# Kernel optimization log

Measured on AMD Instinct MI355X. Metric: run time of the kernel, lower is better.

The kernel has to match this reference:

```python
import jax, jax.numpy as jnp
import numpy as np

N, E, B = 50000, 800000, 128
NF, ED, HID, HEADS, DH, OUT, L = 7, 2, 128, 4, 32, 64, 3
EPS = 1e-5
NEG_SLOPE = 0.2


def _layer_norm(x, g, b):
    mu = jnp.mean(x, axis=-1, keepdims=True)
    v = jnp.mean((x - mu) ** 2, axis=-1, keepdims=True)
    return g * (x - mu) / jnp.sqrt(v + EPS) + b


def setup_inputs() -> dict:
    key = jax.random.key(0)
    ks = jax.random.split(key, 32)
    s = 0.05
    inp = {
        "x": jax.random.normal(ks[0], (N, NF), jnp.float32),
        "edge_index": jax.random.randint(ks[1], (2, E), 0, N, jnp.int32),
        "edge_attr": jax.random.uniform(ks[2], (E, ED), jnp.float32),
        "batch": jnp.sort(jax.random.randint(ks[3], (N,), 0, B, jnp.int32)),
        # node encoder
        "enc_W": jax.random.normal(ks[4], (NF, HID)) * (1.0 / np.sqrt(NF)),
        "enc_b": jnp.zeros((HID,)),
        "enc_g": jnp.ones((HID,)),
        "enc_bb": jnp.zeros((HID,)),
        # GATv2 layers (stacked over L)
        "gat_Wsrc": jax.random.normal(ks[5], (L, HID, HID)) * (1.0 / np.sqrt(HID)),
        "gat_Wdst": jax.random.normal(ks[6], (L, HID, HID)) * (1.0 / np.sqrt(HID)),
        "gat_We": jax.random.normal(ks[7], (L, ED, HID)) * (1.0 / np.sqrt(ED)),
        "gat_att": jax.random.normal(ks[8], (L, HEADS, DH)) * s,
        "gat_bias": jnp.zeros((L, HID)),
        # GraphNorm per layer
        "gn_w": jnp.ones((L, HID)),
        "gn_b": jnp.zeros((L, HID)),
        "gn_s": jnp.ones((L, HID)),  # mean_scale
        # attention pooling
        "pool_W1": jax.random.normal(ks[9], (HID, HID)) * (1.0 / np.sqrt(HID)),
        "pool_b1": jnp.zeros((HID,)),
        "pool_W2": jax.random.normal(ks[10], (HID, 1)) * (1.0 / np.sqrt(HID)),
        # output mapper
        "map_W1": jax.random.normal(ks[11], (HID, HID)) * (1.0 / np.sqrt(HID)),
        "map_b1": jnp.zeros((HID,)),
        "map_g": jnp.ones((HID,)),
        "map_bb": jnp.zeros((HID,)),
        "map_W2": jax.random.normal(ks[12], (HID, OUT)) * (1.0 / np.sqrt(HID)),
        "map_b2": jnp.zeros((OUT,)),
    }
    return inp


def _segment_softmax(scores, seg, num_seg):
    # scores: [E2, HEADS], seg: [E2] destination node ids
    m = jax.ops.segment_max(scores, seg, num_segments=num_seg)
    ex = jnp.exp(scores - m[seg])
    denom = jax.ops.segment_sum(ex, seg, num_segments=num_seg)
    return ex / denom[seg]


def _gatv2(x, src, dst, ea, Wsrc, Wdst, We, att, bias):
    e2 = src.shape[0]
    xl = (x @ Wsrc)[src].reshape(e2, HEADS, DH)   # lin_l(x_j), source
    xr = (x @ Wdst)[dst].reshape(e2, HEADS, DH)   # lin_r(x_i), target
    ee = (ea @ We).reshape(e2, HEADS, DH)
    z = jax.nn.leaky_relu(xl + xr + ee, NEG_SLOPE)
    score = jnp.einsum("ehd,hd->eh", z, att)
    alpha = _segment_softmax(score, dst, N)       # softmax over incoming edges
    msg = (xl * alpha[:, :, None]).reshape(e2, HID)
    out = jax.ops.segment_sum(msg, dst, num_segments=N)
    return out + bias


def _graph_norm(x, batch, w, b, scale):
    cnt = jax.ops.segment_sum(jnp.ones((N,), x.dtype), batch, num_segments=B)
    cnt = jnp.maximum(cnt, 1.0)[:, None]
    mean = jax.ops.segment_sum(x, batch, num_segments=B) / cnt
    xc = x - scale * mean[batch]
    var = jax.ops.segment_sum(xc * xc, batch, num_segments=B) / cnt
    return w * xc / jnp.sqrt(var[batch] + EPS) + b


def reference(x, edge_index, edge_attr, batch, enc_W, enc_b, enc_g, enc_bb,
              gat_Wsrc, gat_Wdst, gat_We, gat_att, gat_bias, gn_w, gn_b, gn_s,
              pool_W1, pool_b1, pool_W2, map_W1, map_b1, map_g, map_bb,
              map_W2, map_b2):
    # node encoder: Linear -> ReLU -> LayerNorm
    h = _layer_norm(jax.nn.relu(x @ enc_W + enc_b), enc_g, enc_bb)

    # add self loops; self-loop edge_attr = mean of edge_attr (PyG fill_value='mean')
    loop = jnp.arange(N, dtype=edge_index.dtype)
    src = jnp.concatenate([edge_index[0], loop])
    dst = jnp.concatenate([edge_index[1], loop])
    ea_mean = jnp.mean(edge_attr, axis=0)
    ea = jnp.concatenate([edge_attr, jnp.broadcast_to(ea_mean, (N, ED))], axis=0)

    for i in range(L):
        out = _gatv2(h, src, dst, ea, gat_Wsrc[i], gat_Wdst[i], gat_We[i],
                     gat_att[i], gat_bias[i])
        out = out + h  # residual (in_dim == out_dim -> Identity proj)
        out = _graph_norm(out, batch, gn_w[i], gn_b[i], gn_s[i])
        h = jax.nn.elu(out)

    node_emb = h
    # attention pooling: softmax over ALL nodes (dim=0, as in source)
    scores = jnp.tanh(h @ pool_W1 + pool_b1) @ pool_W2          # [N, 1]
    weights = jax.nn.softmax(scores, axis=0)
    g = jax.ops.segment_sum(h * weights, batch, num_segments=B)  # [B, HID]

    # output mapper (dropout inactive at eval)
    g = _layer_norm(jax.nn.relu(g @ map_W1 + map_b1), map_g, map_bb)
    graph_emb = g @ map_W2 + map_b2
    return graph_emb, node_emb
```

## Files before the change

kernel.cpp:

```cpp
#include <hip/hip_runtime.h>
#include <hip/hip_bf16.h>

typedef __hip_bfloat16 bf16;
typedef __attribute__((ext_vector_type(8))) short short8;
typedef __attribute__((ext_vector_type(4))) float float4v;

#define Nn   50000
#define Ee   800000
#define E2   850000
#define Bb   128
#define NFd  7
#define HID  128
#define OUTD 64
#define EPS  1e-5f
#define SLOPE 0.2f
#define LOG2E 1.4426950408889634f
#define NSTRIP 3125
#define NPAIR  1563

#define MFMA16(a,b,c) __builtin_amdgcn_mfma_f32_16x16x32_bf16(a,b,c,0,0,0)

__device__ __forceinline__ float lane_bcast(float v, int l){
  return __int_as_float(__builtin_amdgcn_readlane(__float_as_int(v), l));
}
__device__ __forceinline__ float wred_sum(float v){
  #pragma unroll
  for (int o=32;o;o>>=1) v += __shfl_xor(v, o, 64);
  return v;
}
__device__ __forceinline__ float dpp_ror_add(float x, const int ctrl_is_below);
#define DPP_ROR_ADD(x, ctrl) \
  ((x) + __int_as_float(__builtin_amdgcn_update_dpp(0, __float_as_int(x), (ctrl), 0xf, 0xf, false)))
__device__ __forceinline__ float red16_dpp(float x){
  x = DPP_ROR_ADD(x, 0x121);
  x = DPP_ROR_ADD(x, 0x122);
  x = DPP_ROR_ADD(x, 0x124);
  x = DPP_ROR_ADD(x, 0x128);
  return x;
}
__device__ __forceinline__ unsigned fkey(float f){
  unsigned u = __float_as_uint(f);
  return (u & 0x80000000u) ? ~u : (u | 0x80000000u);
}
__device__ __forceinline__ float fkeyinv(unsigned k){
  unsigned u = (k & 0x80000000u) ? (k ^ 0x80000000u) : ~k;
  return __uint_as_float(u);
}
__device__ __forceinline__ float tanh_fast(float x){
  float e = __expf(fminf(fmaxf(2.f*x, -30.f), 30.f));
  return (e-1.f)/(e+1.f);
}
__device__ __forceinline__ float bf_lo(unsigned u){ return __uint_as_float(u<<16); }
__device__ __forceinline__ float bf_hi(unsigned u){ return __uint_as_float(u & 0xffff0000u); }
__device__ __forceinline__ unsigned short f2bs(float f){
  bf16 h = __float2bfloat16(f);
  return *reinterpret_cast<unsigned short*>(&h);
}
__device__ __forceinline__ unsigned pack2(float a, float b){
  return (unsigned)f2bs(a) | ((unsigned)f2bs(b) << 16);
}
__device__ __forceinline__ int xcd_swizzle(int bid, int nwg){
  int q = nwg >> 3, r = nwg & 7;
  int x = bid & 7, i = bid >> 3;
  return (x < r ? x*(q+1) : r*(q+1) + (x-r)*q) + i;
}

__global__ __launch_bounds__(256) void k_encoder(
    const float* __restrict__ x, const float* __restrict__ W, const float* __restrict__ b,
    const float* __restrict__ g, const float* __restrict__ bbv,
    float* __restrict__ h, unsigned* __restrict__ hbu){
  int wv = (blockIdx.x*blockDim.x + threadIdx.x) >> 6;
  if (wv >= Nn) return;
  int lane = threadIdx.x & 63;
  int d0 = 2*lane, d1 = d0+1;
  float y0 = b[d0], y1 = b[d1];
  #pragma unroll
  for (int i=0;i<NFd;++i){
    float xv = x[wv*NFd + i];
    y0 = fmaf(xv, W[i*HID + d0], y0);
    y1 = fmaf(xv, W[i*HID + d1], y1);
  }
  y0 = fmaxf(y0, 0.f); y1 = fmaxf(y1, 0.f);
  float mu = wred_sum(y0+y1) * (1.f/HID);
  float c0 = y0-mu, c1 = y1-mu;
  float var = wred_sum(c0*c0 + c1*c1) * (1.f/HID);
  float rs = rsqrtf(var + EPS);
  float v0 = g[d0]*c0*rs + bbv[d0];
  float v1 = g[d1]*c1*rs + bbv[d1];
  *(float2*)(h + (size_t)wv*HID + d0) = make_float2(v0, v1);
  hbu[(size_t)wv*64 + lane] = pack2(v0, v1);
}

__global__ void k_ea_mean(const float* __restrict__ ea, float* __restrict__ eam){
  int tid = blockIdx.x*blockDim.x + threadIdx.x;
  const float2* ea2 = (const float2*)ea;
  float a0=0.f, a1=0.f;
  for (int e=tid; e<Ee; e += gridDim.x*blockDim.x){
    float2 v = ea2[e];
    a0 += v.x; a1 += v.y;
  }
  a0 = wred_sum(a0); a1 = wred_sum(a1);
  if ((threadIdx.x & 63)==0){
    atomicAdd(&eam[0], a0*(1.f/Ee));
    atomicAdd(&eam[1], a1*(1.f/Ee));
  }
}

__global__ void k_deg(const int* __restrict__ ei, int* __restrict__ deg){
  int e = blockIdx.x*blockDim.x + threadIdx.x;
  if (e >= E2) return;
  int d = (e < Ee) ? ei[Ee + e] : (e - Ee);
  atomicAdd(&deg[d], 1);
}

__global__ __launch_bounds__(1024) void k_scan(const int* __restrict__ deg,
    int* __restrict__ offs, int* __restrict__ cursor){
  __shared__ int wsum[16];
  __shared__ int tot_s;
  __shared__ int carry_s;
  int t = threadIdx.x, lane = t & 63, wid = t >> 6;
  if (t==0) carry_s = 0;
  __syncthreads();
  for (int base=0; base<Nn; base += 4096){
    int i0 = base + t*4;
    int v0=0,v1=0,v2=0,v3=0;
    if (i0+3 < Nn){
      int4 qv = *(const int4*)(deg + i0);
      v0=qv.x; v1=qv.y; v2=qv.z; v3=qv.w;
    } else {
      if (i0   < Nn) v0 = deg[i0];
      if (i0+1 < Nn) v1 = deg[i0+1];
      if (i0+2 < Nn) v2 = deg[i0+2];
      if (i0+3 < Nn) v3 = deg[i0+3];
    }
    int tot = v0+v1+v2+v3;
    int x = tot;
    #pragma unroll
    for (int o=1;o<64;o<<=1){ int u = __shfl_up(x, o, 64); if (lane >= o) x += u; }
    if (lane==63) wsum[wid] = x;
    __syncthreads();
    if (t==0){ int s=0; for (int k=0;k<16;++k){ int tv=wsum[k]; wsum[k]=s; s+=tv; } tot_s = s; }
    __syncthreads();
    int excl = carry_s + wsum[wid] + (x - tot);
    int p0 = excl, p1 = excl+v0, p2 = p1+v1, p3 = p2+v2;
    if (i0+3 < Nn){
      *(int4*)(offs + i0)   = make_int4(p0,p1,p2,p3);
      *(int4*)(cursor + i0) = make_int4(p0,p1,p2,p3);
    } else {
      if (i0   < Nn){ offs[i0]  =p0; cursor[i0]  =p0; }
      if (i0+1 < Nn){ offs[i0+1]=p1; cursor[i0+1]=p1; }
      if (i0+2 < Nn){ offs[i0+2]=p2; cursor[i0+2]=p2; }
      if (i0+3 < Nn){ offs[i0+3]=p3; cursor[i0+3]=p3; }
    }
    __syncthreads();
    if (t==0) carry_s += tot_s;
    __syncthreads();
  }
  if (t==0) offs[Nn] = carry_s;
}

__global__ void k_scatter(const int* __restrict__ ei, const float* __restrict__ ea,
    const float* __restrict__ eam, int* __restrict__ cursor,
    int* __restrict__ csrc, float2* __restrict__ cea){
  int e = blockIdx.x*blockDim.x + threadIdx.x;
  if (e >= E2) return;
  int s, d; float a0, a1;
  if (e < Ee){
    s = ei[e]; d = ei[Ee + e];
    float2 v = ((const float2*)ea)[e];
    a0 = v.x; a1 = v.y;
  } else {
    s = d = e - Ee; a0 = eam[0]; a1 = eam[1];
  }
  int pos = atomicAdd(&cursor[d], 1);
  csrc[pos] = s;
  cea[pos] = make_float2(a0, a1);
}

__global__ void k_gstart(const int* __restrict__ batch, int* __restrict__ gstart){
  int n = blockIdx.x*blockDim.x + threadIdx.x;
  if (n >= Nn) return;
  int bc = batch[n];
  int bp = (n==0) ? -1 : batch[n-1];
  for (int b = bp+1; b <= bc; ++b) gstart[b] = n;
  if (n == Nn-1){ for (int b = bc+1; b <= Bb; ++b) gstart[b] = Nn; }
}

__global__ __launch_bounds__(256) void k_dualgemm(
    const unsigned* __restrict__ hbu,
    const float* __restrict__ Wsrc, const float* __restrict__ Wdst,
    unsigned* __restrict__ hsb, float* __restrict__ hd){
  __shared__ unsigned short wt[256*HID];
  #pragma unroll
  for (int iter=0; iter<64; ++iter){
    int idx = iter*256 + threadIdx.x;
    int n = idx & 255, kp = idx >> 8;
    const float* Wp = (n < 128) ? Wsrc : (Wdst - 128);
    float w0 = Wp[(2*kp)*HID + n];
    float w1 = Wp[(2*kp+1)*HID + n];
    int byt = (n*256 + kp*4) ^ ((n&7)<<4);
    *(unsigned*)((char*)wt + byt) = pack2(w0, w1);
  }
  __syncthreads();
  int wid = threadIdx.x >> 6, lane = threadIdx.x & 63;
  int q = lane >> 4, c = lane & 15;
  const unsigned short* hb = (const unsigned short*)hbu;
  for (int pr = blockIdx.x*4 + wid; pr < NPAIR; pr += gridDim.x*4){
    int p0 = 2*pr, p1 = 2*pr + 1;
    bool v1 = (p1 < NSTRIP);
    int node0 = p0*16 + c;
    int node1 = v1 ? (p1*16 + c) : node0;
    short8 bf0[4], bf1[4];
    const unsigned short* hp0 = hb + (size_t)node0*HID + q*8;
    const unsigned short* hp1 = hb + (size_t)node1*HID + q*8;
    #pragma unroll
    for (int s=0;s<4;++s){
      bf0[s] = *(const short8*)(hp0 + s*32);
      bf1[s] = *(const short8*)(hp1 + s*32);
    }
    #pragma unroll 4
    for (int t=0;t<16;++t){
      float4v ac0 = {0.f,0.f,0.f,0.f}, ac1 = {0.f,0.f,0.f,0.f};
      #pragma unroll
      for (int s=0;s<4;++s){
        int row = t*16 + c;
        int byt = (row*256 + s*64 + q*16) ^ ((row&7)<<4);
        short8 af = *(const short8*)((const char*)wt + byt);
        ac0 = MFMA16(af, bf0[s], ac0);
        ac1 = MFMA16(af, bf1[s], ac1);
      }
      if (t < 8){
        int co = t*8 + q*2;
        *(uint2*)(hsb + (size_t)node0*64 + co) =
            make_uint2(pack2(ac0[0],ac0[1]), pack2(ac0[2],ac0[3]));
        if (v1) *(uint2*)(hsb + (size_t)node1*64 + co) =
            make_uint2(pack2(ac1[0],ac1[1]), pack2(ac1[2],ac1[3]));
      } else {
        int dd = (t-8)*16 + q*4;
        *(float4*)(hd + (size_t)node0*HID + dd) = make_float4(ac0[0],ac0[1],ac0[2],ac0[3]);
        if (v1) *(float4*)(hd + (size_t)node1*HID + dd) = make_float4(ac1[0],ac1[1],ac1[2],ac1[3]);
      }
    }
  }
}

__global__ __launch_bounds__(256) void k_edge(const unsigned* __restrict__ hsb,
    float* __restrict__ hdio, const float* __restrict__ h,
    const int* __restrict__ csrc, const float2* __restrict__ cea,
    const int* __restrict__ offs, const float* __restrict__ We,
    const float* __restrict__ att, const float* __restrict__ bias){
  int bid = xcd_swizzle(blockIdx.x, gridDim.x);
  int n = (bid*256 + (int)threadIdx.x) >> 6;
  if (n >= Nn) return;
  int lane = threadIdx.x & 63;
  int d0 = 2*lane, d1 = d0+1;
  float we00 = We[d0],       we01 = We[d1];
  float we10 = We[HID+d0],   we11 = We[HID+d1];
  float at0  = att[(lane>>4)*32 + (d0&31)] * LOG2E;
  float at1  = att[(lane>>4)*32 + (d1&31)] * LOG2E;
  float2 xr = *(const float2*)(hdio + (size_t)n*HID + d0);
  int e0 = offs[n], e1 = offs[n+1];

  unsigned xu = hsb[((unsigned)csrc[e0]<<6) + lane];
  float2 ev = cea[e0];
  float xl0 = bf_lo(xu), xl1 = bf_hi(xu);
  float z0 = fmaf(ev.y, we10, fmaf(ev.x, we00, xl0 + xr.x));
  float z1 = fmaf(ev.y, we11, fmaf(ev.x, we01, xl1 + xr.y));
  z0 = fmaxf(z0, SLOPE*z0); z1 = fmaxf(z1, SLOPE*z1);
  float m = red16_dpp(fmaf(z1, at1, z0*at0));
  float ssum = 1.f, acc0 = xl0, acc1 = xl1;

  int e = e0 + 1;
  int rem = e1 - e;
  int npair = rem >> 1;
  int sA, sB; float2 eA, eB; unsigned xA, xB;
  if (npair > 0){
    sA = csrc[e]; sB = csrc[e+1];
    eA = cea[e];  eB = cea[e+1];
    xA = hsb[((unsigned)sA<<6) + lane];
    xB = hsb[((unsigned)sB<<6) + lane];
  }
  for (int i = 0; i < npair; ++i){
    int sA_n=0, sB_n=0; float2 eA_n, eB_n; unsigned xA_n=0, xB_n=0;
    if (i+1 < npair){
      int en = e + 2;
      sA_n = csrc[en]; sB_n = csrc[en+1];
      eA_n = cea[en];  eB_n = cea[en+1];
      xA_n = hsb[((unsigned)sA_n<<6) + lane];
      xB_n = hsb[((unsigned)sB_n<<6) + lane];
    }
    float xA0 = bf_lo(xA), xA1 = bf_hi(xA);
    float xB0 = bf_lo(xB), xB1 = bf_hi(xB);
    float zA0 = fmaf(eA.y, we10, fmaf(eA.x, we00, xA0 + xr.x));
    float zA1 = fmaf(eA.y, we11, fmaf(eA.x, we01, xA1 + xr.y));
    float zB0 = fmaf(eB.y, we10, fmaf(eB.x, we00, xB0 + xr.x));
    float zB1 = fmaf(eB.y, we11, fmaf(eB.x, we01, xB1 + xr.y));
    zA0 = fmaxf(zA0, SLOPE*zA0); zA1 = fmaxf(zA1, SLOPE*zA1);
    zB0 = fmaxf(zB0, SLOPE*zB0); zB1 = fmaxf(zB1, SLOPE*zB1);
    float scA = red16_dpp(fmaf(zA1, at1, zA0*at0));
    float scB = red16_dpp(fmaf(zB1, at1, zB0*at0));
    float pA = exp2f(scA - m);
    float pB = exp2f(scB - m);
    ssum += pA + pB;
    acc0 = fmaf(pA, xA0, fmaf(pB, xB0, acc0));
    acc1 = fmaf(pA, xA1, fmaf(pB, xB1, acc1));
    e += 2;
    sA=sA_n; sB=sB_n; eA=eA_n; eB=eB_n; xA=xA_n; xB=xB_n;
  }
  if (rem & 1){
    int s = csrc[e1-1]; float2 eav = cea[e1-1];
    unsigned xt = hsb[((unsigned)s<<6) + lane];
    float x0 = bf_lo(xt), x1 = bf_hi(xt);
    float t0 = fmaf(eav.y, we10, fmaf(eav.x, we00, x0 + xr.x));
    float t1 = fmaf(eav.y, we11, fmaf(eav.x, we01, x1 + xr.y));
    t0 = fmaxf(t0, SLOPE*t0); t1 = fmaxf(t1, SLOPE*t1);
    float sc = red16_dpp(fmaf(t1, at1, t0*at0));
    float p = exp2f(sc - m);
    ssum += p;
    acc0 = fmaf(p, x0, acc0);
    acc1 = fmaf(p, x1, acc1);
  }
  float inv = 1.f/ssum;
  float o0 = acc0*inv + bias[d0] + h[(size_t)n*HID + d0];
  float o1 = acc1*inv + bias[d1] + h[(size_t)n*HID + d1];
  *(float2*)(hdio + (size_t)n*HID + d0) = make_float2(o0, o1);
}

__global__ __launch_bounds__(128) void k_gn_reduce(const float* __restrict__ out,
    const int* __restrict__ gstart, float* __restrict__ gsum_, float* __restrict__ gsq_){
  int b = blockIdx.x >> 4, sub = blockIdx.x & 15;
  int ns = gstart[b], ne = gstart[b+1];
  int d = threadIdx.x;
  float s = 0.f, qq = 0.f;
  for (int n = ns + sub; n < ne; n += 16){
    float v = out[(size_t)n*HID + d];
    s += v; qq = fmaf(v, v, qq);
  }
  atomicAdd(&gsum_[b*HID + d], s);
  atomicAdd(&gsq_[b*HID + d], qq);
}

__global__ __launch_bounds__(256) void k_gn_apply(const float* __restrict__ out,
    const float* __restrict__ gsum_, const float* __restrict__ gsq_,
    const int* __restrict__ gstart, const int* __restrict__ batch,
    const float* __restrict__ gw, const float* __restrict__ gb,
    const float* __restrict__ gs, float* __restrict__ h,
    unsigned* __restrict__ hbu, float* __restrict__ emb){
  int n = (blockIdx.x*blockDim.x + threadIdx.x) >> 6;
  if (n >= Nn) return;
  int lane = threadIdx.x & 63;
  int b = batch[n];
  float icnt = 1.f / fmaxf((float)(gstart[b+1]-gstart[b]), 1.f);
  int d0 = 2*lane, d1 = d0+1;
  float2 x = *(const float2*)(out + (size_t)n*HID + d0);
  float mean0 = gsum_[b*HID+d0]*icnt, mean1 = gsum_[b*HID+d1]*icnt;
  float ms0 = mean0*gs[d0], ms1 = mean1*gs[d1];
  float var0 = gsq_[b*HID+d0]*icnt - ms0*(2.f*mean0 - ms0);
  float var1 = gsq_[b*HID+d1]*icnt - ms1*(2.f*mean1 - ms1);
  float rs0 = rsqrtf(fmaxf(var0, 0.f) + EPS);
  float rs1 = rsqrtf(fmaxf(var1, 0.f) + EPS);
  float y0 = gw[d0]*(x.x - ms0)*rs0 + gb[d0];
  float y1 = gw[d1]*(x.y - ms1)*rs1 + gb[d1];
  y0 = (y0 > 0.f) ? y0 : (__expf(y0) - 1.f);
  y1 = (y1 > 0.f) ? y1 : (__expf(y1) - 1.f);
  *(float2*)(h + (size_t)n*HID + d0) = make_float2(y0, y1);
  hbu[(size_t)n*64 + lane] = pack2(y0, y1);
  if (emb) *(float2*)(emb + (size_t)n*HID + d0) = make_float2(y0, y1);
}

__global__ __launch_bounds__(256) void k_pool_score(
    const unsigned* __restrict__ hbu,
    const float* __restrict__ W1, const float* __restrict__ b1, const float* __restrict__ W2,
    float* __restrict__ score, unsigned* __restrict__ mkey){
  __shared__ unsigned short wt[HID*HID];
  __shared__ float b1l[HID], w2l[HID];
  #pragma unroll
  for (int iter=0; iter<32; ++iter){
    int idx = iter*256 + threadIdx.x;
    int n = idx & 127, kp = idx >> 7;
    float w0 = W1[(2*kp)*HID + n];
    float w1 = W1[(2*kp+1)*HID + n];
    int byt = (n*256 + kp*4) ^ ((n&7)<<4);
    *(unsigned*)((char*)wt + byt) = pack2(w0, w1);
  }
  if (threadIdx.x < HID){ b1l[threadIdx.x] = b1[threadIdx.x]; w2l[threadIdx.x] = W2[threadIdx.x]; }
  __syncthreads();
  int wid = threadIdx.x >> 6, lane = threadIdx.x & 63;
  int q = lane >> 4, c = lane & 15;
  const unsigned short* hb = (const unsigned short*)hbu;
  float bmax = -1e30f;
  for (int p = blockIdx.x*4 + wid; p < NSTRIP; p += gridDim.x*4){
    int node = p*16 + c;
    short8 bf[4];
    const unsigned short* hp = hb + (size_t)node*HID + q*8;
    #pragma unroll
    for (int s=0;s<4;++s) bf[s] = *(const short8*)(hp + s*32);
    float part = 0.f;
    #pragma unroll
    for (int t=0;t<8;++t){
      float4v ac = {0.f,0.f,0.f,0.f};
      #pragma unroll
      for (int s=0;s<4;++s){
        int row = t*16 + c;
        int byt = (row*256 + s*64 + q*16) ^ ((row&7)<<4);
        ac = MFMA16(*(const short8*)((const char*)wt + byt), bf[s], ac);
      }
      int dim = t*16 + q*4;
      #pragma unroll
      for (int r=0;r<4;++r)
        part += tanh_fast(ac[r] + b1l[dim+r]) * w2l[dim+r];
    }
    part += __shfl_xor(part, 16, 64);
    part += __shfl_xor(part, 32, 64);
    if (q==0) score[node] = part;
    bmax = fmaxf(bmax, part);
  }
  #pragma unroll
  for (int o=32;o;o>>=1) bmax = fmaxf(bmax, __shfl_xor(bmax, o, 64));
  if (lane==0) atomicMax(mkey, fkey(bmax));
}

__global__ __launch_bounds__(128) void k_pool_reduce(const float* __restrict__ h,
    const float* __restrict__ score, const unsigned* __restrict__ mkey,
    const int* __restrict__ gstart, float* __restrict__ gsum, float* __restrict__ total){
  int b = blockIdx.x >> 4, sub = blockIdx.x & 15;
  int ns = gstart[b], ne = gstart[b+1];
  float mx = fkeyinv(*mkey);
  int d = threadIdx.x;
  float acc = 0.f, es = 0.f;
  for (int n = ns + sub; n < ne; n += 16){
    float ev = __expf(score[n] - mx);
    acc = fmaf(ev, h[(size_t)n*HID + d], acc);
    if (d==0) es += ev;
  }
  atomicAdd(&gsum[b*HID + d], acc);
  if (d==0) atomicAdd(total, es);
}

__global__ __launch_bounds__(64) void k_mapper(const float* __restrict__ gsum,
    const float* __restrict__ total,
    const float* __restrict__ W1, const float* __restrict__ b1,
    const float* __restrict__ g,  const float* __restrict__ bbv,
    const float* __restrict__ W2, const float* __restrict__ b2v,
    float* __restrict__ out0){
  int b = blockIdx.x, lane = threadIdx.x;
  float inv = 1.f/(*total);
  int d0 = 2*lane, d1 = d0+1;
  float gv0 = gsum[b*HID + d0]*inv, gv1 = gsum[b*HID + d1]*inv;
  float a0 = b1[d0], a1 = b1[d1];
  for (int i=0;i<HID;++i){
    float hv = lane_bcast((i&1) ? gv1 : gv0, i>>1);
    a0 = fmaf(hv, W1[i*HID + d0], a0);
    a1 = fmaf(hv, W1[i*HID + d1], a1);
  }
  a0 = fmaxf(a0, 0.f); a1 = fmaxf(a1, 0.f);
  float mu = wred_sum(a0+a1) * (1.f/HID);
  float c0 = a0-mu, c1 = a1-mu;
  float var = wred_sum(c0*c0 + c1*c1) * (1.f/HID);
  float rs = rsqrtf(var + EPS);
  float l0 = g[d0]*c0*rs + bbv[d0];
  float l1 = g[d1]*c1*rs + bbv[d1];
  float acc = b2v[lane];
  for (int j=0;j<HID;++j){
    float lv = lane_bcast((j&1) ? l1 : l0, j>>1);
    acc = fmaf(lv, W2[j*OUTD + lane], acc);
  }
  out0[b*OUTD + lane] = acc;
}

extern "C" void kernel_launch(void* const* d_in, const int* in_sizes, int n_in,
                              void* d_out, int out_size, void* d_ws, size_t ws_size,
                              hipStream_t stream){
  const float* x     = (const float*)d_in[0];
  const int*   ei    = (const int*)  d_in[1];
  const float* ea    = (const float*)d_in[2];
  const int*   batch = (const int*)  d_in[3];
  const float* encW  = (const float*)d_in[4];
  const float* encb  = (const float*)d_in[5];
  const float* encg  = (const float*)d_in[6];
  const float* encbb = (const float*)d_in[7];
  const float* gWsrc = (const float*)d_in[8];
  const float* gWdst = (const float*)d_in[9];
  const float* gWe   = (const float*)d_in[10];
  const float* gatt  = (const float*)d_in[11];
  const float* gbias = (const float*)d_in[12];
  const float* gnw   = (const float*)d_in[13];
  const float* gnb   = (const float*)d_in[14];
  const float* gns   = (const float*)d_in[15];
  const float* pW1   = (const float*)d_in[16];
  const float* pb1   = (const float*)d_in[17];
  const float* pW2   = (const float*)d_in[18];
  const float* mW1   = (const float*)d_in[19];
  const float* mb1   = (const float*)d_in[20];
  const float* mg    = (const float*)d_in[21];
  const float* mbb   = (const float*)d_in[22];
  const float* mW2   = (const float*)d_in[23];
  const float* mb2   = (const float*)d_in[24];

  char* w = (char*)d_ws;
  size_t off = 0;
  auto alloc = [&](size_t bytes)->char*{
    char* p = w + off;
    off += (bytes + 255) & ~(size_t)255;
    return p;
  };
  float*    h      = (float*)   alloc((size_t)Nn*HID*4);
  unsigned* hbu    = (unsigned*)alloc((size_t)Nn*64*4);
  unsigned* hsb    = (unsigned*)alloc((size_t)Nn*64*4);
  float*    hd     = (float*)   alloc((size_t)Nn*HID*4);
  int*      csrc   = (int*)     alloc((size_t)E2*4);
  float2*   cea    = (float2*)  alloc((size_t)E2*8);
  int*      offs   = (int*)     alloc((size_t)(Nn+1)*4);
  int*      cursor = (int*)     alloc((size_t)Nn*4);
  int*      deg    = (int*)     alloc((size_t)Nn*4);
  int*      gstart = (int*)     alloc((size_t)(Bb+1)*4);
  float*    score  = (float*)   alloc((size_t)Nn*4);
  float*    gsum   = (float*)   alloc((size_t)Bb*HID*4);
  float*    gnsum  = (float*)   alloc((size_t)Bb*HID*4*2);
  float*    scal   = (float*)   alloc(256);
  float*    eam   = scal;
  float*    total = scal + 2;
  unsigned* mkey  = (unsigned*)(scal + 3);
  float*    gnsq  = gnsum + Bb*HID;

  float* out_graph = (float*)d_out;
  float* out_node  = (float*)d_out + (size_t)Bb*OUTD;

  hipMemsetAsync(deg,  0, (size_t)Nn*4, stream);
  hipMemsetAsync(scal, 0, 256, stream);
  hipMemsetAsync(gsum, 0, (size_t)Bb*HID*4, stream);

  k_encoder<<<Nn/4, 256, 0, stream>>>(x, encW, encb, encg, encbb, h, hbu);
  k_ea_mean<<<256, 256, 0, stream>>>(ea, eam);
  k_deg<<<(E2+255)/256, 256, 0, stream>>>(ei, deg);
  k_scan<<<1, 1024, 0, stream>>>(deg, offs, cursor);
  k_scatter<<<(E2+255)/256, 256, 0, stream>>>(ei, ea, eam, cursor, csrc, cea);
  k_gstart<<<(Nn+255)/256, 256, 0, stream>>>(batch, gstart);

  for (int l = 0; l < 3; ++l){
    k_dualgemm<<<256, 256, 0, stream>>>(hbu, gWsrc + (size_t)l*HID*HID,
                                        gWdst + (size_t)l*HID*HID, hsb, hd);
    k_edge<<<Nn/4, 256, 0, stream>>>(hsb, hd, h, csrc, cea, offs,
                                     gWe + (size_t)l*2*HID,
                                     gatt + (size_t)l*4*32,
                                     gbias + (size_t)l*HID);
    hipMemsetAsync(gnsum, 0, (size_t)Bb*HID*4*2, stream);
    k_gn_reduce<<<Bb*16, 128, 0, stream>>>(hd, gstart, gnsum, gnsq);
    k_gn_apply<<<Nn/4, 256, 0, stream>>>(hd, gnsum, gnsq, gstart, batch,
                                         gnw + (size_t)l*HID, gnb + (size_t)l*HID,
                                         gns + (size_t)l*HID, h, hbu,
                                         (l==2) ? out_node : (float*)nullptr);
  }

  k_pool_score<<<256, 256, 0, stream>>>(hbu, pW1, pb1, pW2, score, mkey);
  k_pool_reduce<<<Bb*16, 128, 0, stream>>>(h, score, mkey, gstart, gsum, total);
  k_mapper<<<Bb, 64, 0, stream>>>(gsum, total, mW1, mb1, mg, mbb, mW2, mb2, out_graph);
}
```

Before: 580.0 us.

## Process four edges per wave in GATv2 edge kernel and drop fp32 h buffer

The edge aggregation kernel now handles four edges at a time per wave. Each 16-lane row takes one edge and each lane covers 8 feature dims through a 16-byte bf16 gather. The per-head score reduction becomes a quad DPP sum, and the rows are merged with cross-row shuffles at the end. The fp32 copy of the node features is removed, so the residual add and attention pooling read the packed bf16 buffer instead, which cuts memory traffic but lowers the precision of those paths. The dual GEMM grid is also doubled from 256 to 512 blocks.

```diff
diff --git a/kernel.cpp b/kernel.cpp
--- a/kernel.cpp
+++ b/kernel.cpp
@@ -28,14 +28,11 @@
   for (int o=32;o;o>>=1) v += __shfl_xor(v, o, 64);
   return v;
 }
-__device__ __forceinline__ float dpp_ror_add(float x, const int ctrl_is_below);
-#define DPP_ROR_ADD(x, ctrl) \
-  ((x) + __int_as_float(__builtin_amdgcn_update_dpp(0, __float_as_int(x), (ctrl), 0xf, 0xf, false)))
-__device__ __forceinline__ float red16_dpp(float x){
-  x = DPP_ROR_ADD(x, 0x121);
-  x = DPP_ROR_ADD(x, 0x122);
-  x = DPP_ROR_ADD(x, 0x124);
-  x = DPP_ROR_ADD(x, 0x128);
+#define UPD_DPP(x, ctrl) \
+  __int_as_float(__builtin_amdgcn_update_dpp(0, __float_as_int(x), (ctrl), 0xf, 0xf, false))
+__device__ __forceinline__ float red4_quad(float x){
+  x = x + UPD_DPP(x, 0xB1);
+  x = x + UPD_DPP(x, 0x4E);
   return x;
 }
 __device__ __forceinline__ unsigned fkey(float f){
@@ -68,7 +65,7 @@
 __global__ __launch_bounds__(256) void k_encoder(
     const float* __restrict__ x, const float* __restrict__ W, const float* __restrict__ b,
     const float* __restrict__ g, const float* __restrict__ bbv,
-    float* __restrict__ h, unsigned* __restrict__ hbu){
+    unsigned* __restrict__ hbu){
   int wv = (blockIdx.x*blockDim.x + threadIdx.x) >> 6;
   if (wv >= Nn) return;
   int lane = threadIdx.x & 63;
@@ -87,7 +84,6 @@
   float rs = rsqrtf(var + EPS);
   float v0 = g[d0]*c0*rs + bbv[d0];
   float v1 = g[d1]*c1*rs + bbv[d1];
-  *(float2*)(h + (size_t)wv*HID + d0) = make_float2(v0, v1);
   hbu[(size_t)wv*64 + lane] = pack2(v0, v1);
 }
 
@@ -245,7 +241,7 @@
 }
 
 __global__ __launch_bounds__(256) void k_edge(const unsigned* __restrict__ hsb,
-    float* __restrict__ hdio, const float* __restrict__ h,
+    float* __restrict__ hdio, const unsigned* __restrict__ hbu,
     const int* __restrict__ csrc, const float2* __restrict__ cea,
     const int* __restrict__ offs, const float* __restrict__ We,
     const float* __restrict__ att, const float* __restrict__ bias){
@@ -253,77 +249,80 @@
   int n = (bid*256 + (int)threadIdx.x) >> 6;
   if (n >= Nn) return;
   int lane = threadIdx.x & 63;
-  int d0 = 2*lane, d1 = d0+1;
-  float we00 = We[d0],       we01 = We[d1];
-  float we10 = We[HID+d0],   we11 = We[HID+d1];
-  float at0  = att[(lane>>4)*32 + (d0&31)] * LOG2E;
-  float at1  = att[(lane>>4)*32 + (d1&31)] * LOG2E;
-  float2 xr = *(const float2*)(hdio + (size_t)n*HID + d0);
+  int row = lane >> 4;
+  int c   = lane & 15;
+  int d0  = 8*c;
+  float we0[8], we1[8], at[8], xr[8];
+  #pragma unroll
+  for (int j=0;j<8;++j){
+    we0[j] = We[d0+j];
+    we1[j] = We[HID+d0+j];
+    at[j]  = att[d0+j] * LOG2E;
+  }
+  *(float4*)(xr)   = *(const float4*)(hdio + (size_t)n*HID + d0);
+  *(float4*)(xr+4) = *(const float4*)(hdio + (size_t)n*HID + d0 + 4);
   int e0 = offs[n], e1 = offs[n+1];
-
-  unsigned xu = hsb[((unsigned)csrc[e0]<<6) + lane];
-  float2 ev = cea[e0];
-  float xl0 = bf_lo(xu), xl1 = bf_hi(xu);
-  float z0 = fmaf(ev.y, we10, fmaf(ev.x, we00, xl0 + xr.x));
-  float z1 = fmaf(ev.y, we11, fmaf(ev.x, we01, xl1 + xr.y));
-  z0 = fmaxf(z0, SLOPE*z0); z1 = fmaxf(z1, SLOPE*z1);
-  float m = red16_dpp(fmaf(z1, at1, z0*at0));
-  float ssum = 1.f, acc0 = xl0, acc1 = xl1;
-
-  int e = e0 + 1;
-  int rem = e1 - e;
-  int npair = rem >> 1;
-  int sA, sB; float2 eA, eB; unsigned xA, xB;
-  if (npair > 0){
-    sA = csrc[e]; sB = csrc[e+1];
-    eA = cea[e];  eB = cea[e+1];
-    xA = hsb[((unsigned)sA<<6) + lane];
-    xB = hsb[((unsigned)sB<<6) + lane];
-  }
-  for (int i = 0; i < npair; ++i){
-    int sA_n=0, sB_n=0; float2 eA_n, eB_n; unsigned xA_n=0, xB_n=0;
-    if (i+1 < npair){
-      int en = e + 2;
-      sA_n = csrc[en]; sB_n = csrc[en+1];
-      eA_n = cea[en];  eB_n = cea[en+1];
-      xA_n = hsb[((unsigned)sA_n<<6) + lane];
-      xB_n = hsb[((unsigned)sB_n<<6) + lane];
-    }
-    float xA0 = bf_lo(xA), xA1 = bf_hi(xA);
-    float xB0 = bf_lo(xB), xB1 = bf_hi(xB);
-    float zA0 = fmaf(eA.y, we10, fmaf(eA.x, we00, xA0 + xr.x));
-    float zA1 = fmaf(eA.y, we11, fmaf(eA.x, we01, xA1 + xr.y));
-    float zB0 = fmaf(eB.y, we10, fmaf(eB.x, we00, xB0 + xr.x));
-    float zB1 = fmaf(eB.y, we11, fmaf(eB.x, we01, xB1 + xr.y));
-    zA0 = fmaxf(zA0, SLOPE*zA0); zA1 = fmaxf(zA1, SLOPE*zA1);
-    zB0 = fmaxf(zB0, SLOPE*zB0); zB1 = fmaxf(zB1, SLOPE*zB1);
-    float scA = red16_dpp(fmaf(zA1, at1, zA0*at0));
-    float scB = red16_dpp(fmaf(zB1, at1, zB0*at0));
-    float pA = exp2f(scA - m);
-    float pB = exp2f(scB - m);
-    ssum += pA + pB;
-    acc0 = fmaf(pA, xA0, fmaf(pB, xB0, acc0));
-    acc1 = fmaf(pA, xA1, fmaf(pB, xB1, acc1));
-    e += 2;
-    sA=sA_n; sB=sB_n; eA=eA_n; eB=eB_n; xA=xA_n; xB=xB_n;
-  }
-  if (rem & 1){
-    int s = csrc[e1-1]; float2 eav = cea[e1-1];
-    unsigned xt = hsb[((unsigned)s<<6) + lane];
-    float x0 = bf_lo(xt), x1 = bf_hi(xt);
-    float t0 = fmaf(eav.y, we10, fmaf(eav.x, we00, x0 + xr.x));
-    float t1 = fmaf(eav.y, we11, fmaf(eav.x, we01, x1 + xr.y));
-    t0 = fmaxf(t0, SLOPE*t0); t1 = fmaxf(t1, SLOPE*t1);
-    float sc = red16_dpp(fmaf(t1, at1, t0*at0));
+  float m = 0.f, ssum = 0.f;
+  float acc[8];
+  #pragma unroll
+  for (int j=0;j<8;++j) acc[j] = 0.f;
+
+  int   sC; float2 eC; uint4 xC; bool vC;
+  {
+    int ee = min(e0 + row, E2-1);
+    vC = (e0 + row) < e1;
+    sC = csrc[ee];
+    eC = cea[ee];
+    xC = *(const uint4*)(hsb + ((size_t)(unsigned)sC<<6) + 4*c);
+  }
+  for (int e = e0; e < e1; e += 4){
+    int en = e + 4;
+    int sN=0; float2 eN; uint4 xN; bool vN=false;
+    if (en < e1){
+      int ee = min(en + row, E2-1);
+      vN = (en + row) < e1;
+      sN = csrc[ee];
+      eN = cea[ee];
+      xN = *(const uint4*)(hsb + ((size_t)(unsigned)sN<<6) + 4*c);
+    }
+    float xl[8];
+    xl[0]=bf_lo(xC.x); xl[1]=bf_hi(xC.x); xl[2]=bf_lo(xC.y); xl[3]=bf_hi(xC.y);
+    xl[4]=bf_lo(xC.z); xl[5]=bf_hi(xC.z); xl[6]=bf_lo(xC.w); xl[7]=bf_hi(xC.w);
+    float dot = 0.f;
+    #pragma unroll
+    for (int j=0;j<8;++j){
+      float z = fmaf(eC.y, we1[j], fmaf(eC.x, we0[j], xl[j] + xr[j]));
+      z = fmaxf(z, SLOPE*z);
+      dot = fmaf(z, at[j], dot);
+    }
+    float sc = red4_quad(dot);
+    if (e == e0) m = __shfl(sc, lane & 15, 64);
     float p = exp2f(sc - m);
+    p = vC ? p : 0.f;
     ssum += p;
-    acc0 = fmaf(p, x0, acc0);
-    acc1 = fmaf(p, x1, acc1);
-  }
-  float inv = 1.f/ssum;
-  float o0 = acc0*inv + bias[d0] + h[(size_t)n*HID + d0];
-  float o1 = acc1*inv + bias[d1] + h[(size_t)n*HID + d1];
-  *(float2*)(hdio + (size_t)n*HID + d0) = make_float2(o0, o1);
+    #pragma unroll
+    for (int j=0;j<8;++j) acc[j] = fmaf(p, xl[j], acc[j]);
+    sC=sN; eC=eN; xC=xN; vC=vN;
+  }
+  #pragma unroll
+  for (int j=0;j<8;++j){
+    acc[j] += __shfl_xor(acc[j], 16, 64);
+    acc[j] += __shfl_xor(acc[j], 32, 64);
+  }
+  ssum += __shfl_xor(ssum, 16, 64);
+  ssum += __shfl_xor(ssum, 32, 64);
+  if (row == 0){
+    float inv = 1.f/ssum;
+    uint4 hu = *(const uint4*)(hbu + ((size_t)n<<6) + 4*c);
+    float hr[8];
+    hr[0]=bf_lo(hu.x); hr[1]=bf_hi(hu.x); hr[2]=bf_lo(hu.y); hr[3]=bf_hi(hu.y);
+    hr[4]=bf_lo(hu.z); hr[5]=bf_hi(hu.z); hr[6]=bf_lo(hu.w); hr[7]=bf_hi(hu.w);
+    float o[8];
+    #pragma unroll
+    for (int j=0;j<8;++j) o[j] = fmaf(acc[j], inv, bias[d0+j] + hr[j]);
+    *(float4*)(hdio + (size_t)n*HID + d0)     = make_float4(o[0],o[1],o[2],o[3]);
+    *(float4*)(hdio + (size_t)n*HID + d0 + 4) = make_float4(o[4],o[5],o[6],o[7]);
+  }
 }
 
 __global__ __launch_bounds__(128) void k_gn_reduce(const float* __restrict__ out,
@@ -344,7 +343,7 @@
     const float* __restrict__ gsum_, const float* __restrict__ gsq_,
     const int* __restrict__ gstart, const int* __restrict__ batch,
     const float* __restrict__ gw, const float* __restrict__ gb,
-    const float* __restrict__ gs, float* __restrict__ h,
+    const float* __restrict__ gs,
     unsigned* __restrict__ hbu, float* __restrict__ emb){
   int n = (blockIdx.x*blockDim.x + threadIdx.x) >> 6;
   if (n >= Nn) return;
@@ -363,7 +362,6 @@
   float y1 = gw[d1]*(x.y - ms1)*rs1 + gb[d1];
   y0 = (y0 > 0.f) ? y0 : (__expf(y0) - 1.f);
   y1 = (y1 > 0.f) ? y1 : (__expf(y1) - 1.f);
-  *(float2*)(h + (size_t)n*HID + d0) = make_float2(y0, y1);
   hbu[(size_t)n*64 + lane] = pack2(y0, y1);
   if (emb) *(float2*)(emb + (size_t)n*HID + d0) = make_float2(y0, y1);
 }
@@ -420,7 +418,7 @@
   if (lane==0) atomicMax(mkey, fkey(bmax));
 }
 
-__global__ __launch_bounds__(128) void k_pool_reduce(const float* __restrict__ h,
+__global__ __launch_bounds__(128) void k_pool_reduce(const unsigned* __restrict__ hbu,
     const float* __restrict__ score, const unsigned* __restrict__ mkey,
     const int* __restrict__ gstart, float* __restrict__ gsum, float* __restrict__ total){
   int b = blockIdx.x >> 4, sub = blockIdx.x & 15;
@@ -430,7 +428,9 @@
   float acc = 0.f, es = 0.f;
   for (int n = ns + sub; n < ne; n += 16){
     float ev = __expf(score[n] - mx);
-    acc = fmaf(ev, h[(size_t)n*HID + d], acc);
+    unsigned u = hbu[(size_t)n*64 + (d>>1)];
+    float hv = (d & 1) ? bf_hi(u) : bf_lo(u);
+    acc = fmaf(ev, hv, acc);
     if (d==0) es += ev;
   }
   atomicAdd(&gsum[b*HID + d], acc);
@@ -504,7 +504,6 @@
     off += (bytes + 255) & ~(size_t)255;
     return p;
   };
-  float*    h      = (float*)   alloc((size_t)Nn*HID*4);
   unsigned* hbu    = (unsigned*)alloc((size_t)Nn*64*4);
   unsigned* hsb    = (unsigned*)alloc((size_t)Nn*64*4);
   float*    hd     = (float*)   alloc((size_t)Nn*HID*4);
@@ -530,7 +529,7 @@
   hipMemsetAsync(scal, 0, 256, stream);
   hipMemsetAsync(gsum, 0, (size_t)Bb*HID*4, stream);
 
-  k_encoder<<<Nn/4, 256, 0, stream>>>(x, encW, encb, encg, encbb, h, hbu);
+  k_encoder<<<Nn/4, 256, 0, stream>>>(x, encW, encb, encg, encbb, hbu);
   k_ea_mean<<<256, 256, 0, stream>>>(ea, eam);
   k_deg<<<(E2+255)/256, 256, 0, stream>>>(ei, deg);
   k_scan<<<1, 1024, 0, stream>>>(deg, offs, cursor);
@@ -538,9 +537,9 @@
   k_gstart<<<(Nn+255)/256, 256, 0, stream>>>(batch, gstart);
 
   for (int l = 0; l < 3; ++l){
-    k_dualgemm<<<256, 256, 0, stream>>>(hbu, gWsrc + (size_t)l*HID*HID,
+    k_dualgemm<<<512, 256, 0, stream>>>(hbu, gWsrc + (size_t)l*HID*HID,
                                         gWdst + (size_t)l*HID*HID, hsb, hd);
-    k_edge<<<Nn/4, 256, 0, stream>>>(hsb, hd, h, csrc, cea, offs,
+    k_edge<<<Nn/4, 256, 0, stream>>>(hsb, hd, hbu, csrc, cea, offs,
                                      gWe + (size_t)l*2*HID,
                                      gatt + (size_t)l*4*32,
                                      gbias + (size_t)l*HID);
@@ -548,11 +547,11 @@
     k_gn_reduce<<<Bb*16, 128, 0, stream>>>(hd, gstart, gnsum, gnsq);
     k_gn_apply<<<Nn/4, 256, 0, stream>>>(hd, gnsum, gnsq, gstart, batch,
                                          gnw + (size_t)l*HID, gnb + (size_t)l*HID,
-                                         gns + (size_t)l*HID, h, hbu,
+                                         gns + (size_t)l*HID, hbu,
                                          (l==2) ? out_node : (float*)nullptr);
   }
 
   k_pool_score<<<256, 256, 0, stream>>>(hbu, pW1, pb1, pW2, score, mkey);
-  k_pool_reduce<<<Bb*16, 128, 0, stream>>>(h, score, mkey, gstart, gsum, total);
+  k_pool_reduce<<<Bb*16, 128, 0, stream>>>(hbu, score, mkey, gstart, gsum, total);
   k_mapper<<<Bb, 64, 0, stream>>>(gsum, total, mW1, mb1, mg, mbb, mW2, mb2, out_graph);
 }
```

Result: faster. 537.5 us (-7.3%).
